# Kernel tuning notes

Measured on AMD Instinct MI355X. Metric: run time of the kernel, lower is better.

## Reference

```python
import jax, jax.numpy as jnp
import numpy as np

THRESHOLD = 0.5
NEG_POS_RATIO = 3
ALPHA = 1.0
BETA = 1.0
IGNORE_INDEX = 255

B, P, C, O = 16, 16384, 21, 16
H = W = 256


def cxcy_to_xy(c):
    return jnp.concatenate([c[..., :2] - c[..., 2:] / 2, c[..., :2] + c[..., 2:] / 2], axis=-1)


def xy_to_cxcy(xy):
    return jnp.concatenate([(xy[..., :2] + xy[..., 2:]) / 2, xy[..., 2:] - xy[..., :2]], axis=-1)


def cxcy_to_gcxgcy(cxcy, priors_cxcy):
    return jnp.concatenate([
        (cxcy[..., :2] - priors_cxcy[..., :2]) / (priors_cxcy[..., 2:] / 10.0),
        jnp.log(cxcy[..., 2:] / priors_cxcy[..., 2:]) * 5.0,
    ], axis=-1)


def jaccard(set1, set2):
    # set1 [O,4] xy, set2 [P,4] xy -> IoU [O,P]
    lo = jnp.maximum(set1[:, None, :2], set2[None, :, :2])
    hi = jnp.minimum(set1[:, None, 2:], set2[None, :, 2:])
    wh = jnp.clip(hi - lo, 0.0)
    inter = wh[..., 0] * wh[..., 1]
    a1 = (set1[:, 2] - set1[:, 0]) * (set1[:, 3] - set1[:, 1])
    a2 = (set2[:, 2] - set2[:, 0]) * (set2[:, 3] - set2[:, 1])
    return inter / (a1[:, None] + a2[None, :] - inter)


def setup_inputs() -> dict:
    key = jax.random.key(0)
    ks = jax.random.split(key, 8)
    predicted_locs = jax.random.normal(ks[0], (B, P, 4), dtype=jnp.float32)
    predicted_scores = jax.random.normal(ks[1], (B, P, C), dtype=jnp.float32)
    predicted_masks = jax.random.normal(ks[2], (B, C, H, W), dtype=jnp.float32)
    x1y1 = jax.random.uniform(ks[3], (B, O, 2), dtype=jnp.float32) * 0.8
    wh = jax.random.uniform(ks[4], (B, O, 2), dtype=jnp.float32) * 0.19 + 0.01
    boxes = jnp.concatenate([x1y1, x1y1 + wh], axis=-1)  # valid xy boxes
    pc = jax.random.uniform(ks[5], (P, 2), dtype=jnp.float32) * 0.9 + 0.05
    pwh = jax.random.uniform(ks[6], (P, 2), dtype=jnp.float32) * 0.28 + 0.02
    priors_cxcy = jnp.concatenate([pc, pwh], axis=-1)
    labels = jax.random.randint(ks[7], (B, O), 1, C)  # object labels, never background
    masks = jax.random.randint(jax.random.fold_in(key, 99), (B, 1, H, W), 0, C)
    return {
        'predicted_locs': predicted_locs,
        'predicted_scores': predicted_scores,
        'predicted_masks': predicted_masks,
        'boxes': boxes,
        'priors_cxcy': priors_cxcy,
        'labels': labels,
        'masks': masks,
    }


def _assign(bx, lb, priors_cxcy, priors_xy):
    # bx [O,4] xy, lb [O] int -> true_locs [P,4], true_classes [P]
    ov = jaccard(bx, priors_xy)  # [O,P]
    overlap_for_each_prior = ov.max(axis=0)       # [P]
    object_for_each_prior = ov.argmax(axis=0)     # [P]
    prior_for_each_object = ov.argmax(axis=1)     # [O]
    # guarantee every object is matched to its best prior
    object_for_each_prior = object_for_each_prior.at[prior_for_each_object].set(jnp.arange(O))
    overlap_for_each_prior = overlap_for_each_prior.at[prior_for_each_object].set(1.0)
    label_for_each_prior = lb[object_for_each_prior]
    label_for_each_prior = jnp.where(overlap_for_each_prior < THRESHOLD, 0, label_for_each_prior)
    true_locs = cxcy_to_gcxgcy(xy_to_cxcy(bx[object_for_each_prior]), priors_cxcy)
    return true_locs, label_for_each_prior


def reference(predicted_locs, predicted_scores, predicted_masks, boxes, priors_cxcy, labels, masks):
    priors_xy = cxcy_to_xy(priors_cxcy)
    true_locs, true_classes = jax.vmap(_assign, in_axes=(0, 0, None, None))(
        boxes, labels, priors_cxcy, priors_xy)  # [B,P,4], [B,P]

    pos = true_classes != 0                      # [B,P]
    pos_f = pos.astype(predicted_locs.dtype)
    n_pos = pos.sum(axis=1)                      # [B]

    # localization: L1Loss (mean over positive prior elements)
    diff = jnp.abs(predicted_locs - true_locs)
    loc_loss = (diff * pos_f[..., None]).sum() / jnp.maximum(pos_f.sum() * 4.0, 1.0)

    # confidence: CE per prior + hard negative mining
    logp = jax.nn.log_softmax(predicted_scores, axis=-1)            # [B,P,C]
    ce = -jnp.take_along_axis(logp, true_classes[..., None], axis=-1)[..., 0]  # [B,P]
    ce_pos_sum = (ce * pos_f).sum()
    ce_neg = jnp.where(pos, 0.0, ce)
    ce_neg_sorted = -jnp.sort(-ce_neg, axis=1)                      # descending
    ranks = jnp.arange(P)[None, :]
    hard = (ranks < (NEG_POS_RATIO * n_pos)[:, None]).astype(ce.dtype)
    ce_hardneg_sum = (ce_neg_sorted * hard).sum()
    conf_loss = (ce_hardneg_sum + ce_pos_sum) / n_pos.sum().astype(ce.dtype)

    # mask loss: cross_entropy2d, sum reduction then / (H*W) / B
    tgt = masks[:, 0]                                                # [B,H,W]
    valid = (tgt != IGNORE_INDEX)
    t = jnp.where(valid, tgt, 0)
    logp_m = jax.nn.log_softmax(predicted_masks, axis=1)             # [B,C,H,W]
    ce_m = -jnp.take_along_axis(logp_m, t[:, None], axis=1)[:, 0]    # [B,H,W]
    mask_loss = (ce_m * valid.astype(ce_m.dtype)).sum() / (H * W) / B

    return conf_loss + ALPHA * loc_loss + BETA * mask_loss
```

## Files before the change

### kernel.cpp

```cpp
#include <hip/hip_runtime.h>
#include <cstdint>
#include <cstddef>

#define Bn 16
#define Pn 16384
#define Cn 21
#define On 16
#define HWn 65536
#define THRESH 0.5f


__device__ __forceinline__ float waveReduceSum(float v) {
  for (int off = 32; off > 0; off >>= 1) v += __shfl_down(v, off, 64);
  return v;
}
__device__ __forceinline__ int waveReduceSumI(int v) {
  for (int off = 32; off > 0; off >>= 1) v += __shfl_down(v, off, 64);
  return v;
}

__global__ __launch_bounds__(256) void k_phase1(
    const float* __restrict__ boxes, const float* __restrict__ priors,
    unsigned long long* __restrict__ partials, float* __restrict__ accum,
    int* __restrict__ n_pos, int* __restrict__ n_pos_total,
    int* __restrict__ done_cnt) {
  const int b = blockIdx.x >> 6;
  const int blk = blockIdx.x & 63;
  const int p = (blk << 8) + threadIdx.x;
  if (blockIdx.x == 0) {
    if (threadIdx.x < 4) accum[threadIdx.x] = 0.f;
    if (threadIdx.x < On) n_pos[threadIdx.x] = 0;
    if (threadIdx.x == 32) *n_pos_total = 0;
    if (threadIdx.x == 33) *done_cnt = 0;
  }
  __shared__ float4 sbox[On];
  __shared__ float sarea[On];
  __shared__ unsigned long long skey[On];
  if (threadIdx.x < On) {
    float4 bx = ((const float4*)boxes)[b * On + threadIdx.x];
    sbox[threadIdx.x] = bx;
    sarea[threadIdx.x] = (bx.z - bx.x) * (bx.w - bx.y);
    skey[threadIdx.x] = 0ULL;
  }
  __syncthreads();
  float4 pr = ((const float4*)priors)[p];
  const float px1 = pr.x - 0.5f * pr.z, py1 = pr.y - 0.5f * pr.w;
  const float px2 = pr.x + 0.5f * pr.z, py2 = pr.y + 0.5f * pr.w;
  const float parea = pr.z * pr.w;
  const int lane = threadIdx.x & 63;
#pragma unroll
  for (int o = 0; o < On; ++o) {
    float4 bx = sbox[o];
    float ix = fmaxf(fminf(px2, bx.z) - fmaxf(px1, bx.x), 0.f);
    float iy = fmaxf(fminf(py2, bx.w) - fmaxf(py1, bx.y), 0.f);
    float inter = ix * iy;
    float iou = inter / (sarea[o] + parea - inter);
    unsigned long long key = ((unsigned long long)__float_as_uint(iou) << 32)
                           | (unsigned long long)(0xFFFFFFFFu - (unsigned)p);
    for (int off = 32; off > 0; off >>= 1) {
      unsigned long long other = __shfl_xor(key, off, 64);
      key = key > other ? key : other;
    }
    if (lane == 0) atomicMax(&skey[o], key);
  }
  __syncthreads();
  if (threadIdx.x < On)
    partials[((size_t)blockIdx.x) * On + threadIdx.x] = skey[threadIdx.x];
}

__global__ __launch_bounds__(256, 2) void k_fused(
    const float* __restrict__ plocs, const float* __restrict__ pscores,
    const float* __restrict__ pm, const float* __restrict__ boxes,
    const float* __restrict__ priors, const int* __restrict__ labels,
    const int* __restrict__ msk, const unsigned long long* __restrict__ partials,
    float* __restrict__ ce_neg, float* __restrict__ accum,
    int* __restrict__ n_pos, int* __restrict__ n_pos_total) {
  __shared__ float ssc[256 * Cn];
  __shared__ float4 sbox[On];
  __shared__ float sarea[On];
  __shared__ int slab[On];
  __shared__ int spfo[On];
  __shared__ unsigned long long skey[On];
  __shared__ float sr1[4], sr2[4];
  __shared__ int sri[4];
  const int lane = threadIdx.x & 63, wave = threadIdx.x >> 6;

  if (blockIdx.x < 1024) {
    const int idx4 = blockIdx.x * 256 + threadIdx.x;
    const int b = idx4 >> 14;
    const int pix = (idx4 & 16383) << 2;
    int4 t4 = ((const int4*)msk)[idx4];
    const float* base = pm + (size_t)b * Cn * HWn + pix;
    float4 vv[Cn];
#pragma unroll
    for (int c = 0; c < Cn; ++c)
      vv[c] = *((const float4*)(base + (size_t)c * HWn));
    __builtin_amdgcn_sched_barrier(0);
    const bool v0 = (t4.x != 255), v1 = (t4.y != 255), v2 = (t4.z != 255), v3 = (t4.w != 255);
    const int c0 = v0 ? t4.x : 0, c1 = v1 ? t4.y : 0, c2 = v2 ? t4.z : 0, c3 = v3 ? t4.w : 0;
    float s0 = 0.f, s1 = 0.f, s2 = 0.f, s3 = 0.f;
    float x0 = 0.f, x1 = 0.f, x2 = 0.f, x3 = 0.f;
#pragma unroll
    for (int c = 0; c < Cn; ++c) {
      float4 v = vv[c];
      s0 += __expf(v.x); s1 += __expf(v.y); s2 += __expf(v.z); s3 += __expf(v.w);
      if (c == c0) x0 = v.x;
      if (c == c1) x1 = v.y;
      if (c == c2) x2 = v.z;
      if (c == c3) x3 = v.w;
    }
    float contrib = (v0 ? (__logf(s0) - x0) : 0.f) + (v1 ? (__logf(s1) - x1) : 0.f) +
                    (v2 ? (__logf(s2) - x2) : 0.f) + (v3 ? (__logf(s3) - x3) : 0.f);
    float r = waveReduceSum(contrib);
    if (lane == 0) sr1[wave] = r;
    __syncthreads();
    if (threadIdx.x == 0) atomicAdd(&accum[3], sr1[0] + sr1[1] + sr1[2] + sr1[3]);
    return;
  }

  const int ab = blockIdx.x - 1024;
  const int b = ab >> 6;
  const int p0 = (ab & 63) << 8;
  const int p = p0 + threadIdx.x;
  {
    const float4* src = (const float4*)(pscores + ((size_t)b * Pn + p0) * Cn);
    float4* dst = (float4*)ssc;
#pragma unroll
    for (int i = threadIdx.x; i < (256 * Cn) / 4; i += 256) dst[i] = src[i];
  }
  if (threadIdx.x < On) skey[threadIdx.x] = 0ULL;
  if (threadIdx.x < On) {
    float4 bx = ((const float4*)boxes)[b * On + threadIdx.x];
    sbox[threadIdx.x] = bx;
    sarea[threadIdx.x] = (bx.z - bx.x) * (bx.w - bx.y);
    slab[threadIdx.x] = labels[b * On + threadIdx.x];
  }
  __syncthreads();
  {
    const int o = threadIdx.x & 15, j = threadIdx.x >> 4;
    const unsigned long long* pp = partials + ((size_t)b * 64) * On;
    unsigned long long k = 0ULL;
#pragma unroll
    for (int t = 0; t < 4; ++t) {
      unsigned long long v = pp[(size_t)(j * 4 + t) * On + o];
      k = v > k ? v : k;
    }
    atomicMax(&skey[o], k);
  }
  __syncthreads();
  if (threadIdx.x < On)
    spfo[threadIdx.x] = (int)(0xFFFFFFFFu - (unsigned)(skey[threadIdx.x] & 0xFFFFFFFFULL));
  __syncthreads();

  float4 pr = ((const float4*)priors)[p];
  const float px1 = pr.x - 0.5f * pr.z, py1 = pr.y - 0.5f * pr.w;
  const float px2 = pr.x + 0.5f * pr.z, py2 = pr.y + 0.5f * pr.w;
  const float parea = pr.z * pr.w;
  float best = -1.f;
  int bobj = 0;
#pragma unroll
  for (int o = 0; o < On; ++o) {
    float4 bx = sbox[o];
    float ix = fmaxf(fminf(px2, bx.z) - fmaxf(px1, bx.x), 0.f);
    float iy = fmaxf(fminf(py2, bx.w) - fmaxf(py1, bx.y), 0.f);
    float inter = ix * iy;
    float iou = inter / (sarea[o] + parea - inter);
    if (iou > best) { best = iou; bobj = o; }
  }
#pragma unroll
  for (int o = 0; o < On; ++o) {
    if (spfo[o] == p) { bobj = o; best = 1.0f; }
  }
  const int lbl = (best < THRESH) ? 0 : slab[bobj];
  const bool pos = (lbl != 0);
  float locp = 0.f;
  if (pos) {
    float4 bx = sbox[bobj];
    float cx = 0.5f * (bx.x + bx.z), cy = 0.5f * (bx.y + bx.w);
    float w = bx.z - bx.x, h = bx.w - bx.y;
    float g0 = (cx - pr.x) / (pr.z * 0.1f);
    float g1 = (cy - pr.y) / (pr.w * 0.1f);
    float g2 = logf(w / pr.z) * 5.f;
    float g3 = logf(h / pr.w) * 5.f;
    float4 pl = ((const float4*)plocs)[b * Pn + p];
    locp = fabsf(pl.x - g0) + fabsf(pl.y - g1) + fabsf(pl.z - g2) + fabsf(pl.w - g3);
  }
  const float* my = ssc + threadIdx.x * Cn;
  float s = 0.f, xt = 0.f;
#pragma unroll
  for (int c = 0; c < Cn; ++c) {
    float v = my[c];
    s += __expf(v);
    if (c == lbl) xt = v;
  }
  float ce = __logf(s) - xt;
  ce_neg[b * Pn + p] = pos ? 0.f : ce;
  float cep = pos ? ce : 0.f;

  float r1 = waveReduceSum(locp);
  float r2 = waveReduceSum(cep);
  int ri = waveReduceSumI(pos ? 1 : 0);
  if (lane == 0) { sr1[wave] = r1; sr2[wave] = r2; sri[wave] = ri; }
  __syncthreads();
  if (threadIdx.x == 0) {
    atomicAdd(&accum[0], sr1[0] + sr1[1] + sr1[2] + sr1[3]);
    atomicAdd(&accum[1], sr2[0] + sr2[1] + sr2[2] + sr2[3]);
    int ai = sri[0] + sri[1] + sri[2] + sri[3];
    atomicAdd(&n_pos[b], ai);
    atomicAdd(n_pos_total, ai);
  }
}

__global__ __launch_bounds__(256) void k_hardneg_final(
    const float* __restrict__ ce_neg, const int* __restrict__ n_pos,
    float* __restrict__ accum, const int* __restrict__ n_pos_total,
    int* __restrict__ done_cnt, float* __restrict__ out) {
  const int b = blockIdx.x;
  unsigned rv[64];
#pragma unroll
  for (int i = 0; i < 64; ++i)
    rv[i] = __float_as_uint(ce_neg[b * Pn + i * 256 + threadIdx.x]);
  int K = 3 * n_pos[b];
  if (K > Pn) K = Pn;
  __shared__ int scnt[4];
  __shared__ float ssum[4];
  const int lane = threadIdx.x & 63, wave = threadIdx.x >> 6;
  unsigned lo = 0u, hi = 0x7F800000u;
  while (lo < hi) {
    unsigned mid = lo + ((hi - lo) >> 1);
    int c = 0;
#pragma unroll
    for (int i = 0; i < 64; ++i) c += (rv[i] > mid) ? 1 : 0;
    c = waveReduceSumI(c);
    if (lane == 0) scnt[wave] = c;
    __syncthreads();
    int total = scnt[0] + scnt[1] + scnt[2] + scnt[3];
    if (total < K) hi = mid; else lo = mid + 1;
    __syncthreads();
  }
  const float fv = __uint_as_float(lo);
  float s = 0.f;
  int c = 0;
#pragma unroll
  for (int i = 0; i < 64; ++i) {
    if (rv[i] > lo) { s += __uint_as_float(rv[i]); c++; }
  }
  s = waveReduceSum(s);
  c = waveReduceSumI(c);
  if (lane == 0) { ssum[wave] = s; scnt[wave] = c; }
  __syncthreads();
  if (threadIdx.x == 0) {
    float tots = ssum[0] + ssum[1] + ssum[2] + ssum[3];
    int totc = scnt[0] + scnt[1] + scnt[2] + scnt[3];
    atomicAdd(&accum[2], tots + (float)(K - totc) * fv);
    __threadfence();
    int prev = atomicAdd(done_cnt, 1);
    if (prev == Bn - 1) {
      float a0 = atomicAdd(&accum[0], 0.f);
      float a1 = atomicAdd(&accum[1], 0.f);
      float a2 = atomicAdd(&accum[2], 0.f);
      float a3 = atomicAdd(&accum[3], 0.f);
      float np = (float)(*n_pos_total);
      float conf = (a2 + a1) / np;
      float loc = a0 / fmaxf(np * 4.f, 1.f);
      float maskl = a3 / (float)HWn / (float)Bn;
      out[0] = conf + loc + maskl;
    }
  }
}

extern "C" void kernel_launch(void* const* d_in, const int* in_sizes, int n_in,
                              void* d_out, int out_size, void* d_ws, size_t ws_size,
                              hipStream_t stream) {
  const float* plocs   = (const float*)d_in[0];
  const float* pscores = (const float*)d_in[1];
  const float* pmasks  = (const float*)d_in[2];
  const float* boxes   = (const float*)d_in[3];
  const float* priors  = (const float*)d_in[4];
  const int*   labels  = (const int*)d_in[5];
  const int*   masks   = (const int*)d_in[6];

  char* ws = (char*)d_ws;
  float* accum = (float*)ws;
  int* n_pos = (int*)(ws + 64);
  int* n_pos_total = (int*)(ws + 128);
  int* done_cnt = (int*)(ws + 132);
  unsigned long long* partials = (unsigned long long*)(ws + 4096);
  float* ce_neg = (float*)(ws + 135168);

  k_phase1<<<Bn * 64, 256, 0, stream>>>(boxes, priors, partials, accum, n_pos,
                                        n_pos_total, done_cnt);
  k_fused<<<2048, 256, 0, stream>>>(plocs, pscores, pmasks, boxes, priors,
                                    labels, masks, partials, ce_neg, accum,
                                    n_pos, n_pos_total);
  k_hardneg_final<<<Bn, 256, 0, stream>>>(ce_neg, n_pos, accum, n_pos_total,
                                          done_cnt, (float*)d_out);
}
```

Measured before the change: 231.2 us.

## Move mask loss into first kernel and widen hard-negative selection blocks

The mask cross-entropy blocks move from the assignment kernel into the IoU phase-1 kernel, so the big mask read runs alongside the light IoU work and the assignment kernel gets smaller. The 64-bit shuffle argmax is replaced by a float max reduction plus a ballot that picks the lowest-index tie. The hard-negative radix search now uses 1024-thread blocks with 16 values per thread, which shortens each thread's per-iteration count loop. Accumulator zeroing moves to a hipMemsetAsync, which adds an extra operation on the stream.

Result: no change. 227.2 us (-1.7%).

```diff
diff --git a/kernel.cpp b/kernel.cpp
--- a/kernel.cpp
+++ b/kernel.cpp
@@ -19,23 +19,65 @@
   return v;
 }
 
-__global__ __launch_bounds__(256) void k_phase1(
+__global__ __launch_bounds__(256, 2) void k_p1mask(
     const float* __restrict__ boxes, const float* __restrict__ priors,
-    unsigned long long* __restrict__ partials, float* __restrict__ accum,
-    int* __restrict__ n_pos, int* __restrict__ n_pos_total,
-    int* __restrict__ done_cnt) {
-  const int b = blockIdx.x >> 6;
-  const int blk = blockIdx.x & 63;
-  const int p = (blk << 8) + threadIdx.x;
-  if (blockIdx.x == 0) {
-    if (threadIdx.x < 4) accum[threadIdx.x] = 0.f;
-    if (threadIdx.x < On) n_pos[threadIdx.x] = 0;
-    if (threadIdx.x == 32) *n_pos_total = 0;
-    if (threadIdx.x == 33) *done_cnt = 0;
-  }
+    const float* __restrict__ pm, const int* __restrict__ msk,
+    unsigned long long* __restrict__ partials, float* __restrict__ accum) {
+  const int lane = threadIdx.x & 63, wave = threadIdx.x >> 6;
   __shared__ float4 sbox[On];
   __shared__ float sarea[On];
   __shared__ unsigned long long skey[On];
+  __shared__ float sr1[4];
+
+  if (blockIdx.x >= 1024) {
+    const int idx4 = (blockIdx.x - 1024) * 256 + threadIdx.x;
+    const int b = idx4 >> 14;
+    const int pix = (idx4 & 16383) << 2;
+    int4 t4 = ((const int4*)msk)[idx4];
+    const float* base = pm + (size_t)b * ((size_t)Cn * HWn) + pix;
+#define M_LD(i) float4 v##i = *(const float4*)(base + (size_t)(i) * HWn);
+    M_LD(0) M_LD(1) M_LD(2) M_LD(3) M_LD(4) M_LD(5) M_LD(6) M_LD(7) M_LD(8)
+    M_LD(9) M_LD(10) M_LD(11) M_LD(12) M_LD(13) M_LD(14) M_LD(15) M_LD(16)
+    M_LD(17) M_LD(18) M_LD(19) M_LD(20)
+#undef M_LD
+    asm volatile("" ::"v"(v0.x), "v"(v1.x), "v"(v2.x), "v"(v3.x), "v"(v4.x),
+                 "v"(v5.x), "v"(v6.x), "v"(v7.x), "v"(v8.x), "v"(v9.x),
+                 "v"(v10.x), "v"(v11.x), "v"(v12.x), "v"(v13.x), "v"(v14.x),
+                 "v"(v15.x), "v"(v16.x), "v"(v17.x), "v"(v18.x), "v"(v19.x),
+                 "v"(v20.x));
+    __builtin_amdgcn_sched_barrier(0);
+    const bool q0 = (t4.x != 255), q1 = (t4.y != 255), q2 = (t4.z != 255),
+               q3 = (t4.w != 255);
+    const int c0 = q0 ? t4.x : 0, c1 = q1 ? t4.y : 0, c2 = q2 ? t4.z : 0,
+              c3 = q3 ? t4.w : 0;
+    float s0 = 0.f, s1 = 0.f, s2 = 0.f, s3 = 0.f;
+    float x0 = 0.f, x1 = 0.f, x2 = 0.f, x3 = 0.f;
+#define M_ACC(i)                                                            \
+  {                                                                         \
+    s0 += __expf(v##i.x); s1 += __expf(v##i.y);                             \
+    s2 += __expf(v##i.z); s3 += __expf(v##i.w);                             \
+    if (c0 == i) x0 = v##i.x; if (c1 == i) x1 = v##i.y;                     \
+    if (c2 == i) x2 = v##i.z; if (c3 == i) x3 = v##i.w;                     \
+  }
+    M_ACC(0) M_ACC(1) M_ACC(2) M_ACC(3) M_ACC(4) M_ACC(5) M_ACC(6) M_ACC(7)
+    M_ACC(8) M_ACC(9) M_ACC(10) M_ACC(11) M_ACC(12) M_ACC(13) M_ACC(14)
+    M_ACC(15) M_ACC(16) M_ACC(17) M_ACC(18) M_ACC(19) M_ACC(20)
+#undef M_ACC
+    float contrib = (q0 ? (__logf(s0) - x0) : 0.f) +
+                    (q1 ? (__logf(s1) - x1) : 0.f) +
+                    (q2 ? (__logf(s2) - x2) : 0.f) +
+                    (q3 ? (__logf(s3) - x3) : 0.f);
+    float r = waveReduceSum(contrib);
+    if (lane == 0) sr1[wave] = r;
+    __syncthreads();
+    if (threadIdx.x == 0)
+      atomicAdd(&accum[3], sr1[0] + sr1[1] + sr1[2] + sr1[3]);
+    return;
+  }
+
+  const int b = blockIdx.x >> 6;
+  const int p0 = (blockIdx.x & 63) << 8;
+  const int p = p0 + threadIdx.x;
   if (threadIdx.x < On) {
     float4 bx = ((const float4*)boxes)[b * On + threadIdx.x];
     sbox[threadIdx.x] = bx;
@@ -47,7 +89,6 @@
   const float px1 = pr.x - 0.5f * pr.z, py1 = pr.y - 0.5f * pr.w;
   const float px2 = pr.x + 0.5f * pr.z, py2 = pr.y + 0.5f * pr.w;
   const float parea = pr.z * pr.w;
-  const int lane = threadIdx.x & 63;
 #pragma unroll
   for (int o = 0; o < On; ++o) {
     float4 bx = sbox[o];
@@ -55,24 +96,27 @@
     float iy = fmaxf(fminf(py2, bx.w) - fmaxf(py1, bx.y), 0.f);
     float inter = ix * iy;
     float iou = inter / (sarea[o] + parea - inter);
-    unsigned long long key = ((unsigned long long)__float_as_uint(iou) << 32)
-                           | (unsigned long long)(0xFFFFFFFFu - (unsigned)p);
-    for (int off = 32; off > 0; off >>= 1) {
-      unsigned long long other = __shfl_xor(key, off, 64);
-      key = key > other ? key : other;
+    float m = iou;
+#pragma unroll
+    for (int off = 32; off > 0; off >>= 1) m = fmaxf(m, __shfl_xor(m, off, 64));
+    unsigned long long tie = __ballot(iou == m);
+    if (lane == 0) {
+      int lmin = __ffsll(tie) - 1;
+      unsigned minp = (unsigned)(p0 + (wave << 6) + lmin);
+      unsigned long long key = ((unsigned long long)__float_as_uint(m) << 32) |
+                               (unsigned long long)(0xFFFFFFFFu - minp);
+      atomicMax(&skey[o], key);
     }
-    if (lane == 0) atomicMax(&skey[o], key);
   }
   __syncthreads();
   if (threadIdx.x < On)
-    partials[((size_t)blockIdx.x) * On + threadIdx.x] = skey[threadIdx.x];
-}
-
-__global__ __launch_bounds__(256, 2) void k_fused(
+    partials[(size_t)blockIdx.x * On + threadIdx.x] = skey[threadIdx.x];
+}
+
+__global__ __launch_bounds__(256, 2) void k_assign(
     const float* __restrict__ plocs, const float* __restrict__ pscores,
-    const float* __restrict__ pm, const float* __restrict__ boxes,
-    const float* __restrict__ priors, const int* __restrict__ labels,
-    const int* __restrict__ msk, const unsigned long long* __restrict__ partials,
+    const float* __restrict__ boxes, const float* __restrict__ priors,
+    const int* __restrict__ labels, const unsigned long long* __restrict__ partials,
     float* __restrict__ ce_neg, float* __restrict__ accum,
     int* __restrict__ n_pos, int* __restrict__ n_pos_total) {
   __shared__ float ssc[256 * Cn];
@@ -84,43 +128,8 @@
   __shared__ float sr1[4], sr2[4];
   __shared__ int sri[4];
   const int lane = threadIdx.x & 63, wave = threadIdx.x >> 6;
-
-  if (blockIdx.x < 1024) {
-    const int idx4 = blockIdx.x * 256 + threadIdx.x;
-    const int b = idx4 >> 14;
-    const int pix = (idx4 & 16383) << 2;
-    int4 t4 = ((const int4*)msk)[idx4];
-    const float* base = pm + (size_t)b * Cn * HWn + pix;
-    float4 vv[Cn];
-#pragma unroll
-    for (int c = 0; c < Cn; ++c)
-      vv[c] = *((const float4*)(base + (size_t)c * HWn));
-    __builtin_amdgcn_sched_barrier(0);
-    const bool v0 = (t4.x != 255), v1 = (t4.y != 255), v2 = (t4.z != 255), v3 = (t4.w != 255);
-    const int c0 = v0 ? t4.x : 0, c1 = v1 ? t4.y : 0, c2 = v2 ? t4.z : 0, c3 = v3 ? t4.w : 0;
-    float s0 = 0.f, s1 = 0.f, s2 = 0.f, s3 = 0.f;
-    float x0 = 0.f, x1 = 0.f, x2 = 0.f, x3 = 0.f;
-#pragma unroll
-    for (int c = 0; c < Cn; ++c) {
-      float4 v = vv[c];
-      s0 += __expf(v.x); s1 += __expf(v.y); s2 += __expf(v.z); s3 += __expf(v.w);
-      if (c == c0) x0 = v.x;
-      if (c == c1) x1 = v.y;
-      if (c == c2) x2 = v.z;
-      if (c == c3) x3 = v.w;
-    }
-    float contrib = (v0 ? (__logf(s0) - x0) : 0.f) + (v1 ? (__logf(s1) - x1) : 0.f) +
-                    (v2 ? (__logf(s2) - x2) : 0.f) + (v3 ? (__logf(s3) - x3) : 0.f);
-    float r = waveReduceSum(contrib);
-    if (lane == 0) sr1[wave] = r;
-    __syncthreads();
-    if (threadIdx.x == 0) atomicAdd(&accum[3], sr1[0] + sr1[1] + sr1[2] + sr1[3]);
-    return;
-  }
-
-  const int ab = blockIdx.x - 1024;
-  const int b = ab >> 6;
-  const int p0 = (ab & 63) << 8;
+  const int b = blockIdx.x >> 6;
+  const int p0 = (blockIdx.x & 63) << 8;
   const int p = p0 + threadIdx.x;
   {
     const float4* src = (const float4*)(pscores + ((size_t)b * Pn + p0) * Cn);
@@ -211,30 +220,32 @@
   }
 }
 
-__global__ __launch_bounds__(256) void k_hardneg_final(
+__global__ __launch_bounds__(1024) void k_hardneg_final(
     const float* __restrict__ ce_neg, const int* __restrict__ n_pos,
     float* __restrict__ accum, const int* __restrict__ n_pos_total,
     int* __restrict__ done_cnt, float* __restrict__ out) {
   const int b = blockIdx.x;
-  unsigned rv[64];
-#pragma unroll
-  for (int i = 0; i < 64; ++i)
-    rv[i] = __float_as_uint(ce_neg[b * Pn + i * 256 + threadIdx.x]);
+  const int lane = threadIdx.x & 63, wave = threadIdx.x >> 6;
+  unsigned rv[16];
+#pragma unroll
+  for (int i = 0; i < 16; ++i)
+    rv[i] = __float_as_uint(ce_neg[b * Pn + i * 1024 + threadIdx.x]);
   int K = 3 * n_pos[b];
   if (K > Pn) K = Pn;
-  __shared__ int scnt[4];
-  __shared__ float ssum[4];
-  const int lane = threadIdx.x & 63, wave = threadIdx.x >> 6;
+  __shared__ int scnt[16];
+  __shared__ float ssum[16];
   unsigned lo = 0u, hi = 0x7F800000u;
   while (lo < hi) {
     unsigned mid = lo + ((hi - lo) >> 1);
     int c = 0;
 #pragma unroll
-    for (int i = 0; i < 64; ++i) c += (rv[i] > mid) ? 1 : 0;
+    for (int i = 0; i < 16; ++i) c += (rv[i] > mid) ? 1 : 0;
     c = waveReduceSumI(c);
     if (lane == 0) scnt[wave] = c;
     __syncthreads();
-    int total = scnt[0] + scnt[1] + scnt[2] + scnt[3];
+    int total = 0;
+#pragma unroll
+    for (int w = 0; w < 16; ++w) total += scnt[w];
     if (total < K) hi = mid; else lo = mid + 1;
     __syncthreads();
   }
@@ -242,7 +253,7 @@
   float s = 0.f;
   int c = 0;
 #pragma unroll
-  for (int i = 0; i < 64; ++i) {
+  for (int i = 0; i < 16; ++i) {
     if (rv[i] > lo) { s += __uint_as_float(rv[i]); c++; }
   }
   s = waveReduceSum(s);
@@ -250,8 +261,10 @@
   if (lane == 0) { ssum[wave] = s; scnt[wave] = c; }
   __syncthreads();
   if (threadIdx.x == 0) {
-    float tots = ssum[0] + ssum[1] + ssum[2] + ssum[3];
-    int totc = scnt[0] + scnt[1] + scnt[2] + scnt[3];
+    float tots = 0.f;
+    int totc = 0;
+#pragma unroll
+    for (int w = 0; w < 16; ++w) { tots += ssum[w]; totc += scnt[w]; }
     atomicAdd(&accum[2], tots + (float)(K - totc) * fv);
     __threadfence();
     int prev = atomicAdd(done_cnt, 1);
@@ -288,11 +301,10 @@
   unsigned long long* partials = (unsigned long long*)(ws + 4096);
   float* ce_neg = (float*)(ws + 135168);
 
-  k_phase1<<<Bn * 64, 256, 0, stream>>>(boxes, priors, partials, accum, n_pos,
-                                        n_pos_total, done_cnt);
-  k_fused<<<2048, 256, 0, stream>>>(plocs, pscores, pmasks, boxes, priors,
-                                    labels, masks, partials, ce_neg, accum,
-                                    n_pos, n_pos_total);
-  k_hardneg_final<<<Bn, 256, 0, stream>>>(ce_neg, n_pos, accum, n_pos_total,
-                                          done_cnt, (float*)d_out);
-}
+  (void)hipMemsetAsync(ws, 0, 144, stream);
+  k_p1mask<<<2048, 256, 0, stream>>>(boxes, priors, pmasks, masks, partials, accum);
+  k_assign<<<1024, 256, 0, stream>>>(plocs, pscores, boxes, priors, labels,
+                                     partials, ce_neg, accum, n_pos, n_pos_total);
+  k_hardneg_final<<<Bn, 1024, 0, stream>>>(ce_neg, n_pos, accum, n_pos_total,
+                                           done_cnt, (float*)d_out);
+}
```
